# Kernel tuning notes

Hardware: AMD Instinct MI355X
Metric: run time of the kernel (lower is better)

The kernel has to match this reference:

```python
import jax, jax.numpy as jnp
import numpy as np

EMB = 128
HID = 256
VOCAB = 32000
B, LS, LT = 16, 256, 128


def _lstm(x_seq, h0, c0, Wk, Wr, b):
    """Keras-style LSTM (gate order i,f,g,o). x_seq: [B,T,D] -> ([B,T,H], h, c)."""
    xz = jnp.einsum('btd,dg->btg', x_seq, Wk) + b  # precompute input projection

    def step(carry, zt):
        h, c = carry
        z = zt + h @ Wr  # [B,4H]
        i, f, g, o = jnp.split(z, 4, axis=-1)
        c = jax.nn.sigmoid(f) * c + jax.nn.sigmoid(i) * jnp.tanh(g)
        h = jax.nn.sigmoid(o) * jnp.tanh(c)
        return (h, c), h

    (h, c), hs = jax.lax.scan(step, (h0, c0), xz.transpose(1, 0, 2))
    return hs.transpose(1, 0, 2), h, c


def setup_inputs() -> dict:
    key = jax.random.key(0)
    ks = jax.random.split(key, 12)
    sd_e = 1.0 / np.sqrt(EMB)
    sd_h = 1.0 / np.sqrt(HID)
    return {
        'x': jax.random.randint(ks[0], (B, LS), 0, VOCAB, dtype=jnp.int32),
        'y': jax.random.randint(ks[1], (B, LT), 0, VOCAB, dtype=jnp.int32),
        'enc_emb': jax.random.normal(ks[2], (VOCAB, EMB), jnp.float32) * 0.05,
        'enc_Wk': jax.random.normal(ks[3], (EMB, 4 * HID), jnp.float32) * sd_e,
        'enc_Wr': jax.random.normal(ks[4], (HID, 4 * HID), jnp.float32) * sd_h,
        'enc_b': jnp.zeros((4 * HID,), jnp.float32),
        'dec_emb': jax.random.normal(ks[5], (VOCAB, EMB), jnp.float32) * 0.05,
        'dec_Wk': jax.random.normal(ks[6], (EMB, 4 * HID), jnp.float32) * sd_e,
        'dec_Wr': jax.random.normal(ks[7], (HID, 4 * HID), jnp.float32) * sd_h,
        'dec_b': jnp.zeros((4 * HID,), jnp.float32),
        'Wout': jax.random.normal(ks[8], (2 * HID, VOCAB), jnp.float32) * (1.0 / np.sqrt(2 * HID)),
        'bout': jnp.zeros((VOCAB,), jnp.float32),
    }


def reference(x, y, enc_emb, enc_Wk, enc_Wr, enc_b, dec_emb, dec_Wk, dec_Wr, dec_b, Wout, bout):
    # ---- Encoder ----
    xe = enc_emb[x]  # [B,LS,EMB]
    z0 = jnp.zeros((x.shape[0], HID), jnp.float32)
    H, h, c = _lstm(xe, z0, z0, enc_Wk, enc_Wr, enc_b)  # H: [B,LS,HID]
    # ---- Decoder (teacher forcing) ----
    ye = dec_emb[y]  # [B,LT,EMB]
    S, hT, cT = _lstm(ye, h, c, dec_Wk, dec_Wr, dec_b)  # [B,LT,HID]
    S_ = jnp.concatenate([h[:, None, :], S[:, :-1, :]], axis=1)  # shifted states
    # Keras Attention (dot, no scale): A = softmax(S_ H^T) H
    scores = jnp.einsum('btd,bsd->bts', S_, H)  # [B,LT,LS]
    A = jnp.einsum('bts,bsd->btd', jax.nn.softmax(scores, axis=-1), H)
    feat = jnp.concatenate([S, A], axis=-1)  # [B,LT,2*HID]
    probs = jax.nn.softmax(feat @ Wout + bout, axis=-1)  # [B,LT,VOCAB]
    return probs
```

## Files before the change

### kernel.cpp

```cpp
#include <hip/hip_runtime.h>
#include <hip/hip_bf16.h>
#include <math.h>

#define BB    16
#define LS    256
#define LT    128
#define EMB   128
#define HID   256
#define G4    1024
#define VOCAB 32000

#define NSL   8
#define XROWS 112
#define LSTM_POOL (4096 + XROWS * 128 * 4)

typedef __attribute__((ext_vector_type(8))) short bf16x8;
typedef __attribute__((ext_vector_type(4))) float f32x4;
typedef __attribute__((ext_vector_type(4))) int   i32x4;
typedef unsigned short ushort_t;
typedef unsigned int uint_t;

__device__ inline float sigf(float x)      { return 1.0f / (1.0f + __expf(-x)); }
__device__ inline float tanhfast(float x)  { return 1.0f - 2.0f / (1.0f + __expf(2.0f * x)); }
__device__ inline ushort_t bf16_rne(float f) {
  __hip_bfloat16 h = __float2bfloat16(f);
  return *(ushort_t*)&h;
}

__global__ __launch_bounds__(256) void embed_proj_kernel(
    const int* __restrict__ x, const int* __restrict__ y,
    const float* __restrict__ eemb, const float* __restrict__ eWk,
    const float* __restrict__ eb,
    const float* __restrict__ demb, const float* __restrict__ dWk,
    const float* __restrict__ db,
    float* __restrict__ xze, float* __restrict__ xzd)
{
  const bool enc = blockIdx.x < 128;
  const int* idx = enc ? x : y;
  const float* emb = enc ? eemb : demb;
  const float* Wk  = enc ? eWk  : dWk;
  const float* bias= enc ? eb   : db;
  float* xz        = enc ? xze  : xzd;
  const int row0 = (enc ? blockIdx.x : blockIdx.x - 128) * 32;

  __shared__ float e[32][EMB];
  const int tid = threadIdx.x;

  for (int i = tid; i < 32 * EMB; i += 256) {
    int r = i >> 7, k = i & 127;
    int token = idx[row0 + r];
    e[r][k] = emb[(size_t)token * EMB + k];
  }
  __syncthreads();

  float acc[4][32];
#pragma unroll
  for (int q = 0; q < 4; ++q)
#pragma unroll
    for (int r = 0; r < 32; ++r) acc[q][r] = 0.0f;

  for (int k = 0; k < EMB; ++k) {
    float w0 = Wk[(size_t)k * G4 + 0 * 256 + tid];
    float w1 = Wk[(size_t)k * G4 + 1 * 256 + tid];
    float w2 = Wk[(size_t)k * G4 + 2 * 256 + tid];
    float w3 = Wk[(size_t)k * G4 + 3 * 256 + tid];
#pragma unroll
    for (int r = 0; r < 32; ++r) {
      float ev = e[r][k];
      acc[0][r] = fmaf(ev, w0, acc[0][r]);
      acc[1][r] = fmaf(ev, w1, acc[1][r]);
      acc[2][r] = fmaf(ev, w2, acc[2][r]);
      acc[3][r] = fmaf(ev, w3, acc[3][r]);
    }
  }
#pragma unroll
  for (int q = 0; q < 4; ++q) {
    float bb = bias[q * 256 + tid];
#pragma unroll
    for (int r = 0; r < 32; ++r)
      xz[(size_t)(row0 + r) * G4 + q * 256 + tid] = acc[q][r] + bb;
  }
}

__device__ __forceinline__ void lstm_body(
    char* pool, int bid,
    const float* __restrict__ xz, const float* __restrict__ Wr,
    const float* __restrict__ h0, int h0_stride,
    const float* __restrict__ cinit,
    float* __restrict__ Hout, float* __restrict__ c_fin,
    i32x4* __restrict__ fmb, int kid, int T)
{
  float (*part)[4][128] = (float (*)[4][128])pool;
  float (*xbuf)[128]    = (float (*)[128])(pool + 4096);

  const int b    = bid & (BB - 1);
  const int s    = bid >> 4;
  const int tid  = threadIdx.x;
  const int lane = tid & 63;
  const int quarter = tid >> 7;
  const int col  = tid & 127;
  const int gate = col >> 5, u = col & 31;

  float w_r[64];
  {
    const float* wp = Wr + (size_t)(quarter * 64) * G4 + gate * 256 + s * 32 + u;
#pragma unroll
    for (int j = 0; j < 64; ++j) w_r[j] = wp[(size_t)j * G4];
  }

  const int i0 = quarter * 64 + lane;
  float hv = 0.0f;
  if (h0) hv = h0[(size_t)b * h0_stride + i0];

  float cs0 = 0.0f, cs1 = 0.0f;
  if (tid < 16 && cinit) {
    cs0 = cinit[b * HID + s * 32 + 2 * tid];
    cs1 = cinit[b * HID + s * 32 + 2 * tid + 1];
  }

  const int c0i = i0 >> 1;
  const int sel = i0 & 1;

  int tp = XROWS;
  for (int t = 0; t < T; ++t, ++tp) {
    if (tp >= XROWS) {
      __syncthreads();
      tp = 0;
      for (int tt = quarter; tt < XROWS; tt += 4) {
        int ts = t + tt;
        if (ts < T)
          xbuf[tt][col] = xz[((size_t)b * T + ts) * G4 + gate * 256 + s * 32 + u];
      }
    }

    float a0 = 0.0f, a1 = 0.0f, a2 = 0.0f, a3 = 0.0f;
#pragma unroll
    for (int j = 0; j < 64; j += 4) {
      a0 = fmaf(__int_as_float(__builtin_amdgcn_readlane(__float_as_int(hv), j + 0)), w_r[j + 0], a0);
      a1 = fmaf(__int_as_float(__builtin_amdgcn_readlane(__float_as_int(hv), j + 1)), w_r[j + 1], a1);
      a2 = fmaf(__int_as_float(__builtin_amdgcn_readlane(__float_as_int(hv), j + 2)), w_r[j + 2], a2);
      a3 = fmaf(__int_as_float(__builtin_amdgcn_readlane(__float_as_int(hv), j + 3)), w_r[j + 3], a3);
    }
    part[t & 1][quarter][col] = (a0 + a1) + (a2 + a3);
    __syncthreads();

    const int stamp = (t + 1) | (kid << 20);
    const size_t slot = (size_t)(b * 2 + (t & 1)) * 128;

    if (tid < 16) {
      const int ua = 2 * tid, ub = ua + 1;
      const float (*pp)[128] = part[t & 1];
      float p0a = pp[0][ua] + pp[1][ua] + pp[2][ua] + pp[3][ua];
      float p0b = pp[0][ub] + pp[1][ub] + pp[2][ub] + pp[3][ub];
      float p1a = pp[0][32 + ua] + pp[1][32 + ua] + pp[2][32 + ua] + pp[3][32 + ua];
      float p1b = pp[0][32 + ub] + pp[1][32 + ub] + pp[2][32 + ub] + pp[3][32 + ub];
      float p2a = pp[0][64 + ua] + pp[1][64 + ua] + pp[2][64 + ua] + pp[3][64 + ua];
      float p2b = pp[0][64 + ub] + pp[1][64 + ub] + pp[2][64 + ub] + pp[3][64 + ub];
      float p3a = pp[0][96 + ua] + pp[1][96 + ua] + pp[2][96 + ua] + pp[3][96 + ua];
      float p3b = pp[0][96 + ub] + pp[1][96 + ub] + pp[2][96 + ub] + pp[3][96 + ub];
      float2 xg0 = *(const float2*)&xbuf[tp][ua];
      float2 xg1 = *(const float2*)&xbuf[tp][32 + ua];
      float2 xg2 = *(const float2*)&xbuf[tp][64 + ua];
      float2 xg3 = *(const float2*)&xbuf[tp][96 + ua];

      float zi0 = p0a + xg0.x, zi1 = p0b + xg0.y;
      float zf0 = p1a + xg1.x, zf1 = p1b + xg1.y;
      float zg0 = p2a + xg2.x, zg1 = p2b + xg2.y;
      float zo0 = p3a + xg3.x, zo1 = p3b + xg3.y;

      cs0 = fmaf(sigf(zf0), cs0, sigf(zi0) * tanhfast(zg0));
      cs1 = fmaf(sigf(zf1), cs1, sigf(zi1) * tanhfast(zg1));
      float ha = sigf(zo0) * tanhfast(cs0);
      float hb = sigf(zo1) * tanhfast(cs1);

      *(float2*)&Hout[((size_t)b * T + t) * HID + s * 32 + ua] = make_float2(ha, hb);

      i32x4 ch;
      ch.x = __float_as_int(ha);
      ch.y = __float_as_int(hb);
      ch.z = ch.x ^ ch.y ^ stamp;
      ch.w = 0;
      const i32x4* fd = fmb + slot + s * 16 + tid;
      asm volatile("global_store_dwordx4 %0, %1, off sc0 sc1"
                   :: "v"(fd), "v"(ch) : "memory");
    }
    __syncthreads();

    if (t + 1 < T) {
      const i32x4* fp = fmb + slot + c0i;
      i32x4 va, vb, v;
      asm volatile("global_load_dwordx4 %0, %1, off sc0 sc1"
                   : "=v"(va) : "v"(fp) : "memory");
      asm volatile("global_load_dwordx4 %0, %1, off sc0 sc1"
                   : "=v"(vb) : "v"(fp) : "memory");
      for (;;) {
        asm volatile("s_waitcnt vmcnt(1)" : "+v"(va) :: "memory");
        if (va.z == (va.x ^ va.y ^ stamp)) { v = va; break; }
        asm volatile("global_load_dwordx4 %0, %1, off sc0 sc1"
                     : "=v"(va) : "v"(fp) : "memory");
        asm volatile("s_waitcnt vmcnt(1)" : "+v"(vb) :: "memory");
        if (vb.z == (vb.x ^ vb.y ^ stamp)) { v = vb; break; }
        asm volatile("global_load_dwordx4 %0, %1, off sc0 sc1"
                     : "=v"(vb) : "v"(fp) : "memory");
      }
      asm volatile("s_waitcnt vmcnt(0)" : "+v"(va), "+v"(vb) :: "memory");
      hv = __int_as_float(sel ? v.y : v.x);
    }
  }
  if (c_fin && tid < 16)
    *(float2*)&c_fin[b * HID + s * 32 + 2 * tid] = make_float2(cs0, cs1);
}

__global__ __launch_bounds__(512, 1) void lstm_kernel(
    const float* __restrict__ xz, const float* __restrict__ Wr,
    const float* __restrict__ h0, int h0_stride,
    const float* __restrict__ cinit,
    float* __restrict__ Hout, float* __restrict__ c_fin,
    i32x4* __restrict__ fmb, int kid, int T)
{
  extern __shared__ char pool[];
  lstm_body(pool, blockIdx.x, xz, Wr, h0, h0_stride, cinit,
            Hout, c_fin, fmb, kid, T);
}

__global__ __launch_bounds__(256) void mid_kernel(
    const float* __restrict__ W, ushort_t* __restrict__ WT,
    const float* __restrict__ Henc, const float* __restrict__ S,
    __hip_bfloat16* __restrict__ featB)
{
  const int tid = threadIdx.x;

  if (blockIdx.x < 4000) {
    __shared__ float tile[64][65];
    const int nt = blockIdx.x % 500;
    const int kt = blockIdx.x / 500;
    const int n0 = nt * 64, k0 = kt * 64;
    const int r = tid >> 6, c = tid & 63;

#pragma unroll
    for (int q = 0; q < 16; ++q) {
      int kk = q * 4 + r;
      tile[kk][c] = W[(size_t)(k0 + kk) * VOCAB + n0 + c];
    }
    __syncthreads();

    const int nl = tid >> 2;
    const int seg = (tid & 3) * 16;
    uint_t o[8];
#pragma unroll
    for (int j = 0; j < 8; ++j) {
      uint_t lo = bf16_rne(tile[seg + 2 * j][nl]);
      uint_t hi = bf16_rne(tile[seg + 2 * j + 1][nl]);
      o[j] = lo | (hi << 16);
    }
    ushort_t* dst = WT + (size_t)(n0 + nl) * 512 + k0 + seg;
    ((uint4*)dst)[0] = make_uint4(o[0], o[1], o[2], o[3]);
    ((uint4*)dst)[1] = make_uint4(o[4], o[5], o[6], o[7]);
  } else {
    __shared__ float srow[HID];
    __shared__ float p[LS];
    __shared__ float sm[LS];

    const int m = blockIdx.x - 4000;
    const int b = m >> 7, t = m & (LT - 1);

    const float* s_ = (t == 0) ? (Henc + ((size_t)b * LS + (LS - 1)) * HID)
                               : (S + (size_t)(m - 1) * HID);
    srow[tid] = s_[tid];
    __syncthreads();

    const float4* h4 = (const float4*)(Henc + ((size_t)b * LS + tid) * HID);
    const float4* s4 = (const float4*)srow;
    float sc = 0.0f;
#pragma unroll 8
    for (int k = 0; k < HID / 4; ++k) {
      float4 a = h4[k], q = s4[k];
      sc += a.x * q.x + a.y * q.y + a.z * q.z + a.w * q.w;
    }
    sm[tid] = sc;
    __syncthreads();
    for (int st = 128; st > 0; st >>= 1) {
      if (tid < st) sm[tid] = fmaxf(sm[tid], sm[tid + st]);
      __syncthreads();
    }
    float mx = sm[0];
    __syncthreads();
    float e = __expf(sc - mx);
    p[tid] = e;
    sm[tid] = e;
    __syncthreads();
    for (int st = 128; st > 0; st >>= 1) {
      if (tid < st) sm[tid] += sm[tid + st];
      __syncthreads();
    }
    float inv = 1.0f / sm[0];

    float a_d = 0.0f;
#pragma unroll 4
    for (int s2 = 0; s2 < LS; ++s2)
      a_d = fmaf(p[s2], Henc[((size_t)b * LS + s2) * HID + tid], a_d);
    a_d *= inv;

    featB[(size_t)m * (2 * HID) + tid]       = __float2bfloat16(S[(size_t)m * HID + tid]);
    featB[(size_t)m * (2 * HID) + HID + tid] = __float2bfloat16(a_d);
  }
}

__global__ __launch_bounds__(256) void proj_exp_kernel(
    const ushort_t* __restrict__ A, const ushort_t* __restrict__ BT,
    const float* __restrict__ bout, float* __restrict__ rowsum,
    float* __restrict__ out)
{
  __shared__ ushort_t Ab[2][128 * 64];
  __shared__ ushort_t Bb[2][128 * 64];

  const int bid = blockIdx.x;
  const int k2 = (bid & 7) * 500 + (bid >> 3);
  const int mt = k2 & 15, nt = k2 >> 4;
  const int m0 = mt * 128, n0 = nt * 128;
  const int tid = threadIdx.x;
  const int wave = tid >> 6, lane = tid & 63;
  const int wm = wave >> 1, wn = wave & 1;
  const int r = lane & 15, kg = lane >> 4;

  const ushort_t* Ag = A + (size_t)m0 * 512;
  const ushort_t* Bg = BT + (size_t)n0 * 512;

  f32x4 acc[4][4];
#pragma unroll
  for (int i = 0; i < 4; ++i)
#pragma unroll
    for (int j = 0; j < 4; ++j) acc[i][j] = (f32x4){0.f, 0.f, 0.f, 0.f};

#define STAGE(kc, buf)                                                        \
  {                                                                           \
    _Pragma("unroll")                                                         \
    for (int q = 0; q < 4; ++q) {                                             \
      int L = q * 256 + tid;                                                  \
      int row_ = L >> 3, seg_ = L & 7;                                        \
      int sseg_ = seg_ ^ (row_ & 7);                                          \
      int wbase = (q * 256 + (tid & ~63)) * 8;   \
      __builtin_amdgcn_global_load_lds(                                       \
          (const __attribute__((address_space(1))) unsigned int*)             \
              (Ag + (size_t)row_ * 512 + (kc) * 64 + sseg_ * 8),              \
          (__attribute__((address_space(3))) unsigned int*)&Ab[buf][wbase],   \
          16, 0, 0);                                                          \
      __builtin_amdgcn_global_load_lds(                                       \
          (const __attribute__((address_space(1))) unsigned int*)             \
              (Bg + (size_t)row_ * 512 + (kc) * 64 + sseg_ * 8),              \
          (__attribute__((address_space(3))) unsigned int*)&Bb[buf][wbase],   \
          16, 0, 0);                                                          \
    }                                                                         \
  }

  STAGE(0, 0);
  __syncthreads();

  for (int kc = 0; kc < 8; ++kc) {
    const int cur = kc & 1;
    if (kc < 7) STAGE(kc + 1, cur ^ 1);
#pragma unroll
    for (int ks = 0; ks < 2; ++ks) {
      bf16x8 a[4], b[4];
      const int seg = ks * 4 + kg;
#pragma unroll
      for (int i = 0; i < 4; ++i) {
        int row = wm * 64 + i * 16 + r;
        a[i] = *(const bf16x8*)&Ab[cur][row * 64 + ((seg ^ (row & 7)) << 3)];
      }
#pragma unroll
      for (int j = 0; j < 4; ++j) {
        int row = wn * 64 + j * 16 + r;
        b[j] = *(const bf16x8*)&Bb[cur][row * 64 + ((seg ^ (row & 7)) << 3)];
      }
#pragma unroll
      for (int i = 0; i < 4; ++i)
#pragma unroll
        for (int j = 0; j < 4; ++j)
          acc[i][j] = __builtin_amdgcn_mfma_f32_16x16x32_bf16(a[i], b[j], acc[i][j], 0, 0, 0);
    }
    __syncthreads();
  }
#undef STAGE

  float bv[4];
#pragma unroll
  for (int j = 0; j < 4; ++j) bv[j] = bout[n0 + wn * 64 + j * 16 + r];

#pragma unroll
  for (int i = 0; i < 4; ++i)
#pragma unroll
    for (int q = 0; q < 4; ++q) {
      const int row = m0 + wm * 64 + i * 16 + kg * 4 + q;
      float v = 0.0f;
#pragma unroll
      for (int j = 0; j < 4; ++j) {
        float e = __expf(acc[i][j][q] + bv[j]);
        out[(size_t)row * VOCAB + n0 + wn * 64 + j * 16 + r] = e;
        v += e;
      }
#pragma unroll
      for (int msk = 1; msk < 16; msk <<= 1) v += __shfl_xor(v, msk, 64);
      if (r == 0) atomicAdd(&rowsum[row], v);
    }
}

__global__ __launch_bounds__(256) void scale_kernel(
    float* __restrict__ out, const float* __restrict__ rowsum)
{
  const int row = blockIdx.x >> 2;
  const int seg = blockIdx.x & 3;
  const float s = 1.0f / rowsum[row];
  float4* o4 = (float4*)(out + (size_t)row * VOCAB) + seg * 2000;
  for (int i = threadIdx.x; i < 2000; i += 256) {
    float4 v = o4[i];
    v.x *= s; v.y *= s; v.z *= s; v.w *= s;
    o4[i] = v;
  }
}

extern "C" void kernel_launch(void* const* d_in, const int* in_sizes, int n_in,
                              void* d_out, int out_size, void* d_ws, size_t ws_size,
                              hipStream_t stream) {
  (void)in_sizes; (void)n_in; (void)out_size; (void)ws_size;

  const int*   x       = (const int*)d_in[0];
  const int*   y       = (const int*)d_in[1];
  const float* enc_emb = (const float*)d_in[2];
  const float* enc_Wk  = (const float*)d_in[3];
  const float* enc_Wr  = (const float*)d_in[4];
  const float* enc_b   = (const float*)d_in[5];
  const float* dec_emb = (const float*)d_in[6];
  const float* dec_Wk  = (const float*)d_in[7];
  const float* dec_Wr  = (const float*)d_in[8];
  const float* dec_b   = (const float*)d_in[9];
  const float* Wout    = (const float*)d_in[10];
  const float* bout    = (const float*)d_in[11];
  float* out = (float*)d_out;
  char*  ws  = (char*)d_ws;

  size_t off = 0;
  float* xz_enc = (float*)(ws + off); off += (size_t)BB * LS * G4 * 4;
  float* xz_dec = (float*)(ws + off); off += (size_t)BB * LT * G4 * 4;
  float* Henc   = (float*)(ws + off); off += (size_t)BB * LS * HID * 4;
  float* S      = (float*)(ws + off); off += (size_t)BB * LT * HID * 4;
  __hip_bfloat16* featB = (__hip_bfloat16*)(ws + off);
  off += (size_t)BB * LT * 2 * HID * 2;
  ushort_t* WoutT = (ushort_t*)(ws + off); off += (size_t)VOCAB * 512 * 2;
  float* c_fin  = (float*)(ws + off); off += (size_t)BB * HID * 4;
  size_t zero_base = off;
  float* rowsum = (float*)(ws + off); off += (size_t)BB * LT * 4;
  i32x4* fmb    = (i32x4*)(ws + off); off += (size_t)BB * 2 * 128 * 16;
  size_t zero_len = off - zero_base;

  hipMemsetAsync(ws + zero_base, 0, zero_len, stream);

  embed_proj_kernel<<<192, 256, 0, stream>>>(
      x, y, enc_emb, enc_Wk, enc_b, dec_emb, dec_Wk, dec_b, xz_enc, xz_dec);

  lstm_kernel<<<NSL * BB, 512, LSTM_POOL, stream>>>(
      xz_enc, enc_Wr, nullptr, 0, nullptr, Henc, c_fin, fmb, 0, LS);

  lstm_kernel<<<NSL * BB, 512, LSTM_POOL, stream>>>(
      xz_dec, dec_Wr, Henc + (size_t)(LS - 1) * HID, LS * HID, c_fin,
      S, nullptr, fmb, 1, LT);

  mid_kernel<<<4000 + BB * LT, 256, 0, stream>>>(
      Wout, WoutT, Henc, S, (__hip_bfloat16*)featB);

  proj_exp_kernel<<<16 * 250, 256, 0, stream>>>(
      (const ushort_t*)featB, WoutT, bout, rowsum, out);
  scale_kernel<<<4 * BB * LT, 256, 0, stream>>>(out, rowsum);
}
```

Before: 1.152 ms.

## Process two batch rows per LSTM block, halving block count

Each LSTM block now handles two batch elements (b and b+8) sharing the same register-resident recurrent weight slice, so the grid shrinks from 128 to 64 blocks. The xz staging buffer is split per batch with half the rows each, and two wavefront subsets compute the gate nonlinearities for the two batches in parallel. The double-buffered speculative polling of the flag mailbox is replaced by a simple serial poll per batch. Fewer blocks means fewer participants in the cross-block exchange and less weight traffic, at the cost of twice the FMA work per step on the critical path.

```diff
diff --git a/kernel.cpp b/kernel.cpp
--- a/kernel.cpp
+++ b/kernel.cpp
@@ -11,8 +11,8 @@
 #define VOCAB 32000
 
 #define NSL   8
-#define XROWS 112
-#define LSTM_POOL (4096 + XROWS * 128 * 4)
+#define XROWS 56
+#define LSTM_POOL (4096 + 2 * XROWS * 128 * 4)
 
 typedef __attribute__((ext_vector_type(8))) short bf16x8;
 typedef __attribute__((ext_vector_type(4))) float f32x4;
@@ -91,10 +91,11 @@
     i32x4* __restrict__ fmb, int kid, int T)
 {
   float (*part)[4][128] = (float (*)[4][128])pool;
-  float (*xbuf)[128]    = (float (*)[128])(pool + 4096);
-
-  const int b    = bid & (BB - 1);
-  const int s    = bid >> 4;
+  float (*xbuf)[XROWS][128] = (float (*)[XROWS][128])(pool + 4096);
+
+  const int b0i  = bid & 7;
+  const int b1i  = b0i + 8;
+  const int s    = bid >> 3;
   const int tid  = threadIdx.x;
   const int lane = tid & 63;
   const int quarter = tid >> 7;
@@ -109,13 +110,19 @@
   }
 
   const int i0 = quarter * 64 + lane;
-  float hv = 0.0f;
-  if (h0) hv = h0[(size_t)b * h0_stride + i0];
-
+  float hv0 = 0.0f, hv1 = 0.0f;
+  if (h0) {
+    hv0 = h0[(size_t)b0i * h0_stride + i0];
+    hv1 = h0[(size_t)b1i * h0_stride + i0];
+  }
+
+  const int pw  = (tid < 16) ? 0 : ((tid >= 64 && tid < 80) ? 1 : -1);
+  const int up  = tid & 15;
+  const int mybatch = (pw == 1) ? b1i : b0i;
   float cs0 = 0.0f, cs1 = 0.0f;
-  if (tid < 16 && cinit) {
-    cs0 = cinit[b * HID + s * 32 + 2 * tid];
-    cs1 = cinit[b * HID + s * 32 + 2 * tid + 1];
+  if (pw >= 0 && cinit) {
+    cs0 = cinit[mybatch * HID + s * 32 + 2 * up];
+    cs1 = cinit[mybatch * HID + s * 32 + 2 * up + 1];
   }
 
   const int c0i = i0 >> 1;
@@ -128,28 +135,44 @@
       tp = 0;
       for (int tt = quarter; tt < XROWS; tt += 4) {
         int ts = t + tt;
-        if (ts < T)
-          xbuf[tt][col] = xz[((size_t)b * T + ts) * G4 + gate * 256 + s * 32 + u];
-      }
-    }
-
-    float a0 = 0.0f, a1 = 0.0f, a2 = 0.0f, a3 = 0.0f;
-#pragma unroll
-    for (int j = 0; j < 64; j += 4) {
-      a0 = fmaf(__int_as_float(__builtin_amdgcn_readlane(__float_as_int(hv), j + 0)), w_r[j + 0], a0);
-      a1 = fmaf(__int_as_float(__builtin_amdgcn_readlane(__float_as_int(hv), j + 1)), w_r[j + 1], a1);
-      a2 = fmaf(__int_as_float(__builtin_amdgcn_readlane(__float_as_int(hv), j + 2)), w_r[j + 2], a2);
-      a3 = fmaf(__int_as_float(__builtin_amdgcn_readlane(__float_as_int(hv), j + 3)), w_r[j + 3], a3);
-    }
-    part[t & 1][quarter][col] = (a0 + a1) + (a2 + a3);
+        if (ts < T) {
+          xbuf[0][tt][col] = xz[((size_t)b0i * T + ts) * G4 + gate * 256 + s * 32 + u];
+          xbuf[1][tt][col] = xz[((size_t)b1i * T + ts) * G4 + gate * 256 + s * 32 + u];
+        }
+      }
+    }
+
+    {
+      float a0 = 0.0f, a1 = 0.0f, a2 = 0.0f, a3 = 0.0f;
+#pragma unroll
+      for (int j = 0; j < 64; j += 4) {
+        a0 = fmaf(__int_as_float(__builtin_amdgcn_readlane(__float_as_int(hv0), j + 0)), w_r[j + 0], a0);
+        a1 = fmaf(__int_as_float(__builtin_amdgcn_readlane(__float_as_int(hv0), j + 1)), w_r[j + 1], a1);
+        a2 = fmaf(__int_as_float(__builtin_amdgcn_readlane(__float_as_int(hv0), j + 2)), w_r[j + 2], a2);
+        a3 = fmaf(__int_as_float(__builtin_amdgcn_readlane(__float_as_int(hv0), j + 3)), w_r[j + 3], a3);
+      }
+      part[0][quarter][col] = (a0 + a1) + (a2 + a3);
+    }
+    {
+      float a0 = 0.0f, a1 = 0.0f, a2 = 0.0f, a3 = 0.0f;
+#pragma unroll
+      for (int j = 0; j < 64; j += 4) {
+        a0 = fmaf(__int_as_float(__builtin_amdgcn_readlane(__float_as_int(hv1), j + 0)), w_r[j + 0], a0);
+        a1 = fmaf(__int_as_float(__builtin_amdgcn_readlane(__float_as_int(hv1), j + 1)), w_r[j + 1], a1);
+        a2 = fmaf(__int_as_float(__builtin_amdgcn_readlane(__float_as_int(hv1), j + 2)), w_r[j + 2], a2);
+        a3 = fmaf(__int_as_float(__builtin_amdgcn_readlane(__float_as_int(hv1), j + 3)), w_r[j + 3], a3);
+      }
+      part[1][quarter][col] = (a0 + a1) + (a2 + a3);
+    }
     __syncthreads();
 
     const int stamp = (t + 1) | (kid << 20);
-    const size_t slot = (size_t)(b * 2 + (t & 1)) * 128;
-
-    if (tid < 16) {
-      const int ua = 2 * tid, ub = ua + 1;
-      const float (*pp)[128] = part[t & 1];
+    const size_t slot0 = (size_t)(b0i * 2 + (t & 1)) * 128;
+    const size_t slot1 = (size_t)(b1i * 2 + (t & 1)) * 128;
+
+    if (pw >= 0) {
+      const int ua = 2 * up, ub = ua + 1;
+      const float (*pp)[128] = part[pw];
       float p0a = pp[0][ua] + pp[1][ua] + pp[2][ua] + pp[3][ua];
       float p0b = pp[0][ub] + pp[1][ub] + pp[2][ub] + pp[3][ub];
       float p1a = pp[0][32 + ua] + pp[1][32 + ua] + pp[2][32 + ua] + pp[3][32 + ua];
@@ -158,10 +181,10 @@
       float p2b = pp[0][64 + ub] + pp[1][64 + ub] + pp[2][64 + ub] + pp[3][64 + ub];
       float p3a = pp[0][96 + ua] + pp[1][96 + ua] + pp[2][96 + ua] + pp[3][96 + ua];
       float p3b = pp[0][96 + ub] + pp[1][96 + ub] + pp[2][96 + ub] + pp[3][96 + ub];
-      float2 xg0 = *(const float2*)&xbuf[tp][ua];
-      float2 xg1 = *(const float2*)&xbuf[tp][32 + ua];
-      float2 xg2 = *(const float2*)&xbuf[tp][64 + ua];
-      float2 xg3 = *(const float2*)&xbuf[tp][96 + ua];
+      float2 xg0 = *(const float2*)&xbuf[pw][tp][ua];
+      float2 xg1 = *(const float2*)&xbuf[pw][tp][32 + ua];
+      float2 xg2 = *(const float2*)&xbuf[pw][tp][64 + ua];
+      float2 xg3 = *(const float2*)&xbuf[pw][tp][96 + ua];
 
       float zi0 = p0a + xg0.x, zi1 = p0b + xg0.y;
       float zf0 = p1a + xg1.x, zf1 = p1b + xg1.y;
@@ -173,42 +196,47 @@
       float ha = sigf(zo0) * tanhfast(cs0);
       float hb = sigf(zo1) * tanhfast(cs1);
 
-      *(float2*)&Hout[((size_t)b * T + t) * HID + s * 32 + ua] = make_float2(ha, hb);
+      *(float2*)&Hout[((size_t)mybatch * T + t) * HID + s * 32 + ua] =
+          make_float2(ha, hb);
 
       i32x4 ch;
       ch.x = __float_as_int(ha);
       ch.y = __float_as_int(hb);
       ch.z = ch.x ^ ch.y ^ stamp;
       ch.w = 0;
-      const i32x4* fd = fmb + slot + s * 16 + tid;
+      const i32x4* fd = fmb + (pw ? slot1 : slot0) + s * 16 + up;
       asm volatile("global_store_dwordx4 %0, %1, off sc0 sc1"
                    :: "v"(fd), "v"(ch) : "memory");
     }
     __syncthreads();
 
     if (t + 1 < T) {
-      const i32x4* fp = fmb + slot + c0i;
-      i32x4 va, vb, v;
-      asm volatile("global_load_dwordx4 %0, %1, off sc0 sc1"
-                   : "=v"(va) : "v"(fp) : "memory");
-      asm volatile("global_load_dwordx4 %0, %1, off sc0 sc1"
-                   : "=v"(vb) : "v"(fp) : "memory");
-      for (;;) {
-        asm volatile("s_waitcnt vmcnt(1)" : "+v"(va) :: "memory");
-        if (va.z == (va.x ^ va.y ^ stamp)) { v = va; break; }
-        asm volatile("global_load_dwordx4 %0, %1, off sc0 sc1"
-                     : "=v"(va) : "v"(fp) : "memory");
-        asm volatile("s_waitcnt vmcnt(1)" : "+v"(vb) :: "memory");
-        if (vb.z == (vb.x ^ vb.y ^ stamp)) { v = vb; break; }
-        asm volatile("global_load_dwordx4 %0, %1, off sc0 sc1"
-                     : "=v"(vb) : "v"(fp) : "memory");
-      }
-      asm volatile("s_waitcnt vmcnt(0)" : "+v"(va), "+v"(vb) :: "memory");
-      hv = __int_as_float(sel ? v.y : v.x);
-    }
-  }
-  if (c_fin && tid < 16)
-    *(float2*)&c_fin[b * HID + s * 32 + 2 * tid] = make_float2(cs0, cs1);
+      {
+        const i32x4* fp = fmb + slot0 + c0i;
+        i32x4 v;
+        for (;;) {
+          asm volatile("global_load_dwordx4 %0, %1, off sc0 sc1\n\t"
+                       "s_waitcnt vmcnt(0)"
+                       : "=&v"(v) : "v"(fp) : "memory");
+          if (v.z == (v.x ^ v.y ^ stamp)) break;
+        }
+        hv0 = __int_as_float(sel ? v.y : v.x);
+      }
+      {
+        const i32x4* fp = fmb + slot1 + c0i;
+        i32x4 v;
+        for (;;) {
+          asm volatile("global_load_dwordx4 %0, %1, off sc0 sc1\n\t"
+                       "s_waitcnt vmcnt(0)"
+                       : "=&v"(v) : "v"(fp) : "memory");
+          if (v.z == (v.x ^ v.y ^ stamp)) break;
+        }
+        hv1 = __int_as_float(sel ? v.y : v.x);
+      }
+    }
+  }
+  if (c_fin && pw >= 0)
+    *(float2*)&c_fin[mybatch * HID + s * 32 + 2 * up] = make_float2(cs0, cs1);
 }
 
 __global__ __launch_bounds__(512, 1) void lstm_kernel(
@@ -458,10 +486,10 @@
   embed_proj_kernel<<<192, 256, 0, stream>>>(
       x, y, enc_emb, enc_Wk, enc_b, dec_emb, dec_Wk, dec_b, xz_enc, xz_dec);
 
-  lstm_kernel<<<NSL * BB, 512, LSTM_POOL, stream>>>(
+  lstm_kernel<<<NSL * 8, 512, LSTM_POOL, stream>>>(
       xz_enc, enc_Wr, nullptr, 0, nullptr, Henc, c_fin, fmb, 0, LS);
 
-  lstm_kernel<<<NSL * BB, 512, LSTM_POOL, stream>>>(
+  lstm_kernel<<<NSL * 8, 512, LSTM_POOL, stream>>>(
       xz_dec, dec_Wr, Henc + (size_t)(LS - 1) * HID, LS * HID, c_fin,
       S, nullptr, fmb, 1, LT);
 
```

Result: slower. 1.580 ms (+37.2%).
